# Performance work log

Measured on AMD Instinct MI355X. Metric: run time of the kernel, lower is better.

Reference implementation:

```python
import jax, jax.numpy as jnp
import numpy as np

VOCAB = 100000
D = 128
B = 256
L = 2048  # leaves per tree (power of two -> complete binary tree)


def setup_inputs() -> dict:
    key = jax.random.key(0)
    k1, k2, k3, k4 = jax.random.split(key, 4)
    word_ids = jax.random.randint(k1, (B, L), 0, VOCAB)
    embedding = jax.random.normal(k2, (VOCAB, D), dtype=jnp.float32) * 0.1
    # torch nn.Linear(2*D, D): weight [D, 2*D], bias [D]
    W = jax.random.normal(k3, (D, 2 * D), dtype=jnp.float32) * (1.0 / np.sqrt(2 * D))
    b = jax.random.normal(k4, (D,), dtype=jnp.float32) * 0.01
    return {"word_ids": word_ids, "embedding": embedding, "W": W, "b": b}


def reference(word_ids, embedding, W, b):
    # Leaves: embedding lookup for every leaf of every tree. [B, L, D]
    x = embedding[word_ids]
    # Internal nodes, batched by depth: each level combines adjacent pairs
    # via linear(concat(left, right)). log2(L) levels (static unroll).
    while x.shape[1] > 1:
        left = x[:, 0::2, :]   # [B, n/2, D]
        right = x[:, 1::2, :]  # [B, n/2, D]
        pair = jnp.concatenate([left, right], axis=-1)  # [B, n/2, 2D]
        x = jnp.einsum('bnd,od->bno', pair, W) + b      # [B, n/2, D]
    return x[:, 0, :]  # root result per tree, [B, D]
```

## Files before the change

### kernel.cpp

```cpp
#include <hip/hip_runtime.h>


typedef __bf16 bf16x8 __attribute__((ext_vector_type(8)));
typedef __bf16 bf16x4 __attribute__((ext_vector_type(4)));
typedef float f32x4 __attribute__((ext_vector_type(4)));

#define STRIDE 136

__global__ void prep_kernel(const float* __restrict__ W,
                            const float* __restrict__ emb,
                            __bf16* __restrict__ wpack,
                            __bf16* __restrict__ etab, int n8) {
    const int tid = threadIdx.x;
    if (blockIdx.x < 16) {
        const int f = blockIdx.x;
        const int wv = tid >> 6, l = tid & 63;
        const int nl = f >> 3, kk = f & 7;
        const int o = ((wv << 1) + nl) * 16 + (l & 15);
        const int d = kk * 32 + ((l >> 4) << 3);
        const float* src = W + o * 256 + d;
        bf16x8 h;
#pragma unroll
        for (int j = 0; j < 8; ++j) h[j] = (__bf16)src[j];
        *(bf16x8*)(wpack + (size_t)(f * 256 + tid) * 8) = h;
    }
    const int stride = gridDim.x * blockDim.x;
    for (int i = blockIdx.x * blockDim.x + tid; i < n8; i += stride) {
        const float* s = emb + (size_t)i * 8;
        const f32x4 a = *(const f32x4*)s;
        const f32x4 b = *(const f32x4*)(s + 4);
        const bf16x4 ha = __builtin_convertvector(a, bf16x4);
        const bf16x4 hb = __builtin_convertvector(b, bf16x4);
        bf16x8 h;
#pragma unroll
        for (int j = 0; j < 4; ++j) { h[j] = ha[j]; h[4 + j] = hb[j]; }
        *(bf16x8*)(etab + (size_t)i * 8) = h;
    }
}

__device__ __forceinline__ void step32(
    const __bf16* src0, const __bf16* src1, __bf16* dst,
    const bf16x8* wf, const float* bval, int wv, int q, int lm)
{
    f32x4 acc[2][2];
#pragma unroll
    for (int mt = 0; mt < 2; ++mt)
#pragma unroll
        for (int nl = 0; nl < 2; ++nl)
            acc[mt][nl] = f32x4{ bval[nl], bval[nl], bval[nl], bval[nl] };
#pragma unroll
    for (int kh = 0; kh < 2; ++kh) {
        const int row = 2 * lm + kh;
        bf16x8 a0[4], a1[4];
#pragma unroll
        for (int j = 0; j < 4; ++j) {
            a0[j] = *(const bf16x8*)&src0[row * STRIDE + j * 32 + q * 8];
            a1[j] = *(const bf16x8*)&src1[row * STRIDE + j * 32 + q * 8];
        }
#pragma unroll
        for (int j = 0; j < 4; ++j) {
            acc[0][0] = __builtin_amdgcn_mfma_f32_16x16x32_bf16(
                a0[j], wf[0 * 8 + kh * 4 + j], acc[0][0], 0, 0, 0);
            acc[1][0] = __builtin_amdgcn_mfma_f32_16x16x32_bf16(
                a1[j], wf[0 * 8 + kh * 4 + j], acc[1][0], 0, 0, 0);
            acc[0][1] = __builtin_amdgcn_mfma_f32_16x16x32_bf16(
                a0[j], wf[1 * 8 + kh * 4 + j], acc[0][1], 0, 0, 0);
            acc[1][1] = __builtin_amdgcn_mfma_f32_16x16x32_bf16(
                a1[j], wf[1 * 8 + kh * 4 + j], acc[1][1], 0, 0, 0);
        }
    }
#pragma unroll
    for (int mt = 0; mt < 2; ++mt)
#pragma unroll
        for (int nl = 0; nl < 2; ++nl) {
            const int col = (2 * wv + nl) * 16 + lm;
            const bf16x4 hv = __builtin_convertvector(acc[mt][nl], bf16x4);
#pragma unroll
            for (int r = 0; r < 4; ++r)
                dst[(mt * 16 + q * 4 + r) * STRIDE + col] = hv[r];
        }
    __syncthreads();
}

template <int NOUT>
__device__ __forceinline__ void step_small(
    const __bf16* src, __bf16* dst,
    const bf16x8* wf, const float* bval, int wv, int q, int lm)
{
    const int me = (NOUT >= 16) ? lm : (lm < NOUT ? lm : 0);
    f32x4 acc[2];
    acc[0] = f32x4{ bval[0], bval[0], bval[0], bval[0] };
    acc[1] = f32x4{ bval[1], bval[1], bval[1], bval[1] };
#pragma unroll
    for (int kh = 0; kh < 2; ++kh) {
        const int row = 2 * me + kh;
        bf16x8 af[4];
#pragma unroll
        for (int j = 0; j < 4; ++j)
            af[j] = *(const bf16x8*)&src[row * STRIDE + j * 32 + q * 8];
#pragma unroll
        for (int nl = 0; nl < 2; ++nl)
#pragma unroll
            for (int j = 0; j < 4; ++j)
                acc[nl] = __builtin_amdgcn_mfma_f32_16x16x32_bf16(
                    af[j], wf[nl * 8 + kh * 4 + j], acc[nl], 0, 0, 0);
    }
#pragma unroll
    for (int nl = 0; nl < 2; ++nl) {
        const int col = (2 * wv + nl) * 16 + lm;
        const bf16x4 hv = __builtin_convertvector(acc[nl], bf16x4);
#pragma unroll
        for (int r = 0; r < 4; ++r) {
            const int row = q * 4 + r;
            if (row < NOUT)
                dst[row * STRIDE + col] = hv[r];
        }
    }
    __syncthreads();
}

__device__ __forceinline__ void final4(
    const __bf16* src, __bf16* yrow,
    const bf16x8* wf, const float* bval, int wv, int q, int lm)
{
    const int me = (lm < 4) ? lm : 0;
    f32x4 acc[2];
    acc[0] = f32x4{ bval[0], bval[0], bval[0], bval[0] };
    acc[1] = f32x4{ bval[1], bval[1], bval[1], bval[1] };
#pragma unroll
    for (int kh = 0; kh < 2; ++kh) {
        const int row = 2 * me + kh;
        bf16x8 af[4];
#pragma unroll
        for (int j = 0; j < 4; ++j)
            af[j] = *(const bf16x8*)&src[row * STRIDE + j * 32 + q * 8];
#pragma unroll
        for (int nl = 0; nl < 2; ++nl)
#pragma unroll
            for (int j = 0; j < 4; ++j)
                acc[nl] = __builtin_amdgcn_mfma_f32_16x16x32_bf16(
                    af[j], wf[nl * 8 + kh * 4 + j], acc[nl], 0, 0, 0);
    }
#pragma unroll
    for (int nl = 0; nl < 2; ++nl) {
        const int col = (2 * wv + nl) * 16 + lm;
        if (q == 0) {
#pragma unroll
            for (int r = 0; r < 4; ++r)
                yrow[r * 128 + col] = (__bf16)acc[nl][r];
        }
    }
}

__device__ __forceinline__ void gather_issue_f32(
    const int* wb64, const float* emb, int tid, f32x4 (&s)[8])
{
#pragma unroll
    for (int i = 0; i < 8; ++i) {
        const int id = wb64[(tid >> 5) + 8 * i];
        s[i] = *(const f32x4*)(emb + (size_t)id * 128 + (tid & 31) * 4);
    }
}
__device__ __forceinline__ void gather_write_f32(
    __bf16* dst, int tid, const f32x4 (&s)[8])
{
#pragma unroll
    for (int i = 0; i < 8; ++i) {
        const int row = (tid >> 5) + 8 * i;
        *(bf16x4*)&dst[row * STRIDE + (tid & 31) * 4] =
            __builtin_convertvector(s[i], bf16x4);
    }
}

__device__ __forceinline__ void gather_issue_bf(
    const int* wb64, const __bf16* etab, int tid, bf16x4 (&s)[8])
{
#pragma unroll
    for (int i = 0; i < 8; ++i) {
        const int id = wb64[(tid >> 5) + 8 * i];
        s[i] = *(const bf16x4*)(etab + (size_t)id * 128 + (tid & 31) * 4);
    }
}
__device__ __forceinline__ void gather_write_bf(
    __bf16* dst, int tid, const bf16x4 (&s)[8])
{
#pragma unroll
    for (int i = 0; i < 8; ++i) {
        const int row = (tid >> 5) + 8 * i;
        *(bf16x4*)&dst[row * STRIDE + (tid & 31) * 4] = s[i];
    }
}

template <bool BF>
__global__ __launch_bounds__(256, 3) void tree128_kernel(
    const int* __restrict__ wid, const float* __restrict__ emb,
    const __bf16* __restrict__ etab, const __bf16* __restrict__ wpack,
    const float* __restrict__ bias, __bf16* __restrict__ yout)
{
    __shared__ __align__(16) __bf16 bufA[64 * STRIDE];
    __shared__ __align__(16) __bf16 bufB[64 * STRIDE];
    __shared__ __align__(16) __bf16 bufD[64 * STRIDE];
    const int tid = threadIdx.x;
    const int batch = blockIdx.x >> 3;
    const int pair = blockIdx.x & 7;
    const int wv = tid >> 6, ln = tid & 63, q = ln >> 4, lm = ln & 15;

    bf16x8 wf[16];
    const bf16x8* wp = (const bf16x8*)wpack;
#pragma unroll
    for (int f = 0; f < 16; ++f) wf[f] = wp[f * 256 + tid];
    float bval[2];
    bval[0] = bias[(2 * wv + 0) * 16 + lm];
    bval[1] = bias[(2 * wv + 1) * 16 + lm];

    const int* wb = wid + batch * 2048 + pair * 256;
    f32x4 st32[8];
    bf16x4 st16[8];

    auto issue = [&](const int* p) {
        if constexpr (BF) gather_issue_bf(p, etab, tid, st16);
        else              gather_issue_f32(p, emb, tid, st32);
    };
    auto write = [&](__bf16* d) {
        if constexpr (BF) gather_write_bf(d, tid, st16);
        else              gather_write_f32(d, tid, st32);
    };

    issue(wb);
    write(bufA);
    __syncthreads();
    issue(wb + 64);
    step32(bufA, bufA + 32 * STRIDE, bufB, wf, bval, wv, q, lm);
    write(bufA);
    __syncthreads();
    issue(wb + 128);
    step32(bufA, bufA + 32 * STRIDE, bufB + 32 * STRIDE, wf, bval, wv, q, lm);
    write(bufA);
    step32(bufB, bufB + 32 * STRIDE, bufD, wf, bval, wv, q, lm);
    issue(wb + 192);
    step32(bufA, bufA + 32 * STRIDE, bufB, wf, bval, wv, q, lm);
    write(bufA);
    __syncthreads();
    step32(bufA, bufA + 32 * STRIDE, bufB + 32 * STRIDE, wf, bval, wv, q, lm);
    step32(bufB, bufB + 32 * STRIDE, bufD + 32 * STRIDE, wf, bval, wv, q, lm);
    step32(bufD, bufD + 32 * STRIDE, bufB, wf, bval, wv, q, lm);
    step_small<16>(bufB, bufD, wf, bval, wv, q, lm);
    step_small<8>(bufD, bufB, wf, bval, wv, q, lm);
    final4(bufB, yout + (size_t)(batch * 32 + pair * 4) * 128,
           wf, bval, wv, q, lm);
}

__global__ __launch_bounds__(256) void tree32_kernel(
    const __bf16* __restrict__ yin, const __bf16* __restrict__ wpack,
    const float* __restrict__ bias, float* __restrict__ out)
{
    __shared__ __align__(16) __bf16 buf0[32 * STRIDE];
    __shared__ __align__(16) __bf16 buf1[16 * STRIDE];
    const int tid = threadIdx.x;
    const int batch = blockIdx.x;
    const int wv = tid >> 6, ln = tid & 63, q = ln >> 4, lm = ln & 15;

    bf16x8 wf[16];
    const bf16x8* wp = (const bf16x8*)wpack;
#pragma unroll
    for (int f = 0; f < 16; ++f) wf[f] = wp[f * 256 + tid];
    float bval[2];
    bval[0] = bias[(2 * wv + 0) * 16 + lm];
    bval[1] = bias[(2 * wv + 1) * 16 + lm];

#pragma unroll
    for (int i = 0; i < 2; ++i) {
        const int flat = tid + 256 * i;
        const int row = flat >> 4;
        const int c8 = flat & 15;
        const bf16x8 v =
            *(const bf16x8*)(yin + (size_t)(batch * 32 + row) * 128 + c8 * 8);
        *(bf16x8*)&buf0[row * STRIDE + c8 * 8] = v;
    }
    __syncthreads();

    step_small<16>(buf0, buf1, wf, bval, wv, q, lm);
    step_small<8> (buf1, buf0, wf, bval, wv, q, lm);
    step_small<4> (buf0, buf1, wf, bval, wv, q, lm);
    step_small<2> (buf1, buf0, wf, bval, wv, q, lm);

    {
        f32x4 acc[2];
        acc[0] = f32x4{ bval[0], bval[0], bval[0], bval[0] };
        acc[1] = f32x4{ bval[1], bval[1], bval[1], bval[1] };
#pragma unroll
        for (int kh = 0; kh < 2; ++kh) {
            bf16x8 af[4];
#pragma unroll
            for (int j = 0; j < 4; ++j)
                af[j] = *(const bf16x8*)&buf0[kh * STRIDE + j * 32 + q * 8];
#pragma unroll
            for (int nl = 0; nl < 2; ++nl)
#pragma unroll
                for (int j = 0; j < 4; ++j)
                    acc[nl] = __builtin_amdgcn_mfma_f32_16x16x32_bf16(
                        af[j], wf[nl * 8 + kh * 4 + j], acc[nl], 0, 0, 0);
        }
#pragma unroll
        for (int nl = 0; nl < 2; ++nl) {
            const int col = (2 * wv + nl) * 16 + lm;
            if (q == 0) out[(size_t)batch * 128 + col] = acc[nl][0];
        }
    }
}

extern "C" void kernel_launch(void* const* d_in, const int* in_sizes, int n_in,
                              void* d_out, int out_size, void* d_ws, size_t ws_size,
                              hipStream_t stream) {
    const int*   wid = (const int*)d_in[0];
    const float* emb = (const float*)d_in[1];
    const float* W   = (const float*)d_in[2];
    const float* b   = (const float*)d_in[3];
    float* out = (float*)d_out;

    __bf16* wpack = (__bf16*)d_ws;
    __bf16* y     = wpack + 32768;
    __bf16* etab  = y + 256 * 32 * 128;

    const size_t need = (size_t)32768 * 2 + (size_t)256 * 32 * 128 * 2
                      + (size_t)100000 * 128 * 2;
    const bool bf = (ws_size >= need);
    const int n8 = bf ? (100000 * 128 / 8) : 0;

    prep_kernel<<<bf ? 2048 : 16, 256, 0, stream>>>(W, emb, wpack, etab, n8);
    if (bf)
        tree128_kernel<true><<<2048, 256, 0, stream>>>(
            wid, emb, etab, wpack, b, y);
    else
        tree128_kernel<false><<<2048, 256, 0, stream>>>(
            wid, emb, etab, wpack, b, y);
    tree32_kernel<<<256, 256, 0, stream>>>(y, wpack, b, out);
}
```

Before: 131.8 us.

## Prefetch word ids, double-buffer bf16 gathers, and use lightweight LDS barriers

The bf16 gather path now preloads all word ids up front and keeps two register stages of 16-byte gathers in flight, so each embedding gather overlaps with more MFMA work. The old per-step __syncthreads is replaced by an explicit barrier that waits only on LDS counters, letting outstanding global loads stay in flight across barriers. Barrier placement moves to the call sites. The cost is higher register pressure from the extra staging buffers and preloaded ids, which at three blocks per SM could cause spills.

```diff
diff --git a/kernel.cpp b/kernel.cpp
--- a/kernel.cpp
+++ b/kernel.cpp
@@ -6,6 +6,11 @@
 typedef float f32x4 __attribute__((ext_vector_type(4)));
 
 #define STRIDE 136
+
+#define BARRIER() do {                                          \
+    asm volatile("s_waitcnt lgkmcnt(0)" ::: "memory");          \
+    __builtin_amdgcn_s_barrier();                               \
+} while (0)
 
 __global__ void prep_kernel(const float* __restrict__ W,
                             const float* __restrict__ emb,
@@ -79,7 +84,6 @@
             for (int r = 0; r < 4; ++r)
                 dst[(mt * 16 + q * 4 + r) * STRIDE + col] = hv[r];
         }
-    __syncthreads();
 }
 
 template <int NOUT>
@@ -116,7 +120,6 @@
                 dst[row * STRIDE + col] = hv[r];
         }
     }
-    __syncthreads();
 }
 
 __device__ __forceinline__ void final4(
@@ -152,7 +155,24 @@
     }
 }
 
-__device__ __forceinline__ void gather_issue_f32(
+__device__ __forceinline__ void gissue_bf(
+    const int (&ids)[4], const __bf16* etab, int tid, bf16x8 (&s)[4])
+{
+#pragma unroll
+    for (int i = 0; i < 4; ++i)
+        s[i] = *(const bf16x8*)(etab + (size_t)ids[i] * 128 + (tid & 15) * 8);
+}
+__device__ __forceinline__ void gwrite_bf(
+    __bf16* dst, int tid, const bf16x8 (&s)[4])
+{
+#pragma unroll
+    for (int i = 0; i < 4; ++i) {
+        const int row = (tid >> 4) + 16 * i;
+        *(bf16x8*)&dst[row * STRIDE + (tid & 15) * 8] = s[i];
+    }
+}
+
+__device__ __forceinline__ void gissue_f32(
     const int* wb64, const float* emb, int tid, f32x4 (&s)[8])
 {
 #pragma unroll
@@ -161,7 +181,7 @@
         s[i] = *(const f32x4*)(emb + (size_t)id * 128 + (tid & 31) * 4);
     }
 }
-__device__ __forceinline__ void gather_write_f32(
+__device__ __forceinline__ void gwrite_f32(
     __bf16* dst, int tid, const f32x4 (&s)[8])
 {
 #pragma unroll
@@ -169,25 +189,6 @@
         const int row = (tid >> 5) + 8 * i;
         *(bf16x4*)&dst[row * STRIDE + (tid & 31) * 4] =
             __builtin_convertvector(s[i], bf16x4);
-    }
-}
-
-__device__ __forceinline__ void gather_issue_bf(
-    const int* wb64, const __bf16* etab, int tid, bf16x4 (&s)[8])
-{
-#pragma unroll
-    for (int i = 0; i < 8; ++i) {
-        const int id = wb64[(tid >> 5) + 8 * i];
-        s[i] = *(const bf16x4*)(etab + (size_t)id * 128 + (tid & 31) * 4);
-    }
-}
-__device__ __forceinline__ void gather_write_bf(
-    __bf16* dst, int tid, const bf16x4 (&s)[8])
-{
-#pragma unroll
-    for (int i = 0; i < 8; ++i) {
-        const int row = (tid >> 5) + 8 * i;
-        *(bf16x4*)&dst[row * STRIDE + (tid & 31) * 4] = s[i];
     }
 }
 
@@ -214,38 +215,69 @@
     bval[1] = bias[(2 * wv + 1) * 16 + lm];
 
     const int* wb = wid + batch * 2048 + pair * 256;
-    f32x4 st32[8];
-    bf16x4 st16[8];
-
-    auto issue = [&](const int* p) {
-        if constexpr (BF) gather_issue_bf(p, etab, tid, st16);
-        else              gather_issue_f32(p, emb, tid, st32);
-    };
-    auto write = [&](__bf16* d) {
-        if constexpr (BF) gather_write_bf(d, tid, st16);
-        else              gather_write_f32(d, tid, st32);
-    };
-
-    issue(wb);
-    write(bufA);
-    __syncthreads();
-    issue(wb + 64);
-    step32(bufA, bufA + 32 * STRIDE, bufB, wf, bval, wv, q, lm);
-    write(bufA);
-    __syncthreads();
-    issue(wb + 128);
-    step32(bufA, bufA + 32 * STRIDE, bufB + 32 * STRIDE, wf, bval, wv, q, lm);
-    write(bufA);
-    step32(bufB, bufB + 32 * STRIDE, bufD, wf, bval, wv, q, lm);
-    issue(wb + 192);
-    step32(bufA, bufA + 32 * STRIDE, bufB, wf, bval, wv, q, lm);
-    write(bufA);
-    __syncthreads();
-    step32(bufA, bufA + 32 * STRIDE, bufB + 32 * STRIDE, wf, bval, wv, q, lm);
+
+    if constexpr (BF) {
+        int ids[4][4];
+#pragma unroll
+        for (int g = 0; g < 4; ++g)
+#pragma unroll
+            for (int i = 0; i < 4; ++i)
+                ids[g][i] = wb[g * 64 + (tid >> 4) + 16 * i];
+
+        bf16x8 s1[4], s2[4];
+        gissue_bf(ids[0], etab, tid, s1);
+        gissue_bf(ids[1], etab, tid, s2);
+        gwrite_bf(bufA, tid, s1);
+        BARRIER();
+        gissue_bf(ids[2], etab, tid, s1);
+        step32(bufA, bufA + 32 * STRIDE, bufB, wf, bval, wv, q, lm);
+        BARRIER();
+        gwrite_bf(bufA, tid, s2);
+        BARRIER();
+        gissue_bf(ids[3], etab, tid, s2);
+        step32(bufA, bufA + 32 * STRIDE, bufB + 32 * STRIDE, wf, bval, wv, q, lm);
+        BARRIER();
+        gwrite_bf(bufA, tid, s1);
+        step32(bufB, bufB + 32 * STRIDE, bufD, wf, bval, wv, q, lm);
+        BARRIER();
+        step32(bufA, bufA + 32 * STRIDE, bufB, wf, bval, wv, q, lm);
+        BARRIER();
+        gwrite_bf(bufA, tid, s2);
+        BARRIER();
+        step32(bufA, bufA + 32 * STRIDE, bufB + 32 * STRIDE, wf, bval, wv, q, lm);
+        BARRIER();
+    } else {
+        f32x4 st[8];
+        gissue_f32(wb, emb, tid, st);
+        gwrite_f32(bufA, tid, st);
+        BARRIER();
+        gissue_f32(wb + 64, emb, tid, st);
+        step32(bufA, bufA + 32 * STRIDE, bufB, wf, bval, wv, q, lm);
+        BARRIER();
+        gwrite_f32(bufA, tid, st);
+        BARRIER();
+        gissue_f32(wb + 128, emb, tid, st);
+        step32(bufA, bufA + 32 * STRIDE, bufB + 32 * STRIDE, wf, bval, wv, q, lm);
+        BARRIER();
+        gwrite_f32(bufA, tid, st);
+        step32(bufB, bufB + 32 * STRIDE, bufD, wf, bval, wv, q, lm);
+        BARRIER();
+        step32(bufA, bufA + 32 * STRIDE, bufB, wf, bval, wv, q, lm);
+        BARRIER();
+        gissue_f32(wb + 192, emb, tid, st);
+        gwrite_f32(bufA, tid, st);
+        BARRIER();
+        step32(bufA, bufA + 32 * STRIDE, bufB + 32 * STRIDE, wf, bval, wv, q, lm);
+        BARRIER();
+    }
     step32(bufB, bufB + 32 * STRIDE, bufD + 32 * STRIDE, wf, bval, wv, q, lm);
+    BARRIER();
     step32(bufD, bufD + 32 * STRIDE, bufB, wf, bval, wv, q, lm);
+    BARRIER();
     step_small<16>(bufB, bufD, wf, bval, wv, q, lm);
+    BARRIER();
     step_small<8>(bufD, bufB, wf, bval, wv, q, lm);
+    BARRIER();
     final4(bufB, yout + (size_t)(batch * 32 + pair * 4) * 128,
            wf, bval, wv, q, lm);
 }
@@ -279,10 +311,10 @@
     }
     __syncthreads();
 
-    step_small<16>(buf0, buf1, wf, bval, wv, q, lm);
-    step_small<8> (buf1, buf0, wf, bval, wv, q, lm);
-    step_small<4> (buf0, buf1, wf, bval, wv, q, lm);
-    step_small<2> (buf1, buf0, wf, bval, wv, q, lm);
+    step_small<16>(buf0, buf1, wf, bval, wv, q, lm);  __syncthreads();
+    step_small<8> (buf1, buf0, wf, bval, wv, q, lm);  __syncthreads();
+    step_small<4> (buf0, buf1, wf, bval, wv, q, lm);  __syncthreads();
+    step_small<2> (buf1, buf0, wf, bval, wv, q, lm);  __syncthreads();
 
     {
         f32x4 acc[2];
```

New measurement: 130.7 us. About the same (-0.8%).
